# Optimization experiments

Measured on AMD Instinct MI355X. Metric: run time of the kernel, lower is better.

The kernel has to match this reference:

```python
import jax, jax.numpy as jnp
import numpy as np

B, T, D, H, C = 64, 512, 128, 512, 256  # batch, seq_len, input_dim, rnn_dim, clf hidden


def _lstm_cell(x, h, c, Wih, Whh, b):
    # PyTorch gate order: i, f, g, o; b = bias_ih + bias_hh
    gates = x @ Wih.T + h @ Whh.T + b  # [B, 4H]
    i, f, g, o = jnp.split(gates, 4, axis=-1)
    c = jax.nn.sigmoid(f) * c + jax.nn.sigmoid(i) * jnp.tanh(g)
    h = jax.nn.sigmoid(o) * jnp.tanh(c)
    return h, c


def _run_lstm2(xs, state, p0, p1):
    # xs: [B, T, in]; state: (h0, c0, h1, c1) each [B, H]
    def step(carry, x_t):
        h0, c0, h1, c1 = carry
        h0, c0 = _lstm_cell(x_t, h0, c0, *p0)
        h1, c1 = _lstm_cell(h0, h1, c1, *p1)
        return (h0, c0, h1, c1), h1
    state, ys = jax.lax.scan(step, state, jnp.swapaxes(xs, 0, 1))
    return jnp.swapaxes(ys, 0, 1), state


def setup_inputs() -> dict:
    key = jax.random.key(0)
    ks = jax.random.split(key, 18)
    s = 0.04  # ~1/sqrt(H), matches torch LSTM init scale
    w = lambda k, shape: (jax.random.normal(k, shape, jnp.float32) * s)
    inp = {
        "x": jax.random.uniform(ks[0], (B, T, D), dtype=jnp.float32),
        "y": (jax.random.uniform(ks[1], (B, T, D), dtype=jnp.float32) > 0.9).astype(jnp.float32),
        "enc_Wih0": w(ks[2], (4 * H, D)), "enc_Whh0": w(ks[3], (4 * H, H)), "enc_b0": w(ks[4], (4 * H,)),
        "enc_Wih1": w(ks[5], (4 * H, H)), "enc_Whh1": w(ks[6], (4 * H, H)), "enc_b1": w(ks[7], (4 * H,)),
        "dec_Wih0": w(ks[8], (4 * H, D)), "dec_Whh0": w(ks[9], (4 * H, H)), "dec_b0": w(ks[10], (4 * H,)),
        "dec_Wih1": w(ks[11], (4 * H, H)), "dec_Whh1": w(ks[12], (4 * H, H)), "dec_b1": w(ks[13], (4 * H,)),
        "clf_W1": w(ks[14], (C, H)), "clf_b1": w(ks[15], (C,)),
        "clf_W2": w(ks[16], (D, C)), "clf_b2": w(ks[17], (D,)),
    }
    return inp


def reference(x, y, enc_Wih0, enc_Whh0, enc_b0, enc_Wih1, enc_Whh1, enc_b1,
              dec_Wih0, dec_Whh0, dec_b0, dec_Wih1, dec_Whh1, dec_b1,
              clf_W1, clf_b1, clf_W2, clf_b2):
    Bc = x.shape[0]
    z = jnp.zeros((Bc, H), x.dtype)
    # encoder: only final (h, c) of both layers is used
    _, state = _run_lstm2(x, (z, z, z, z),
                          (enc_Wih0, enc_Whh0, enc_b0), (enc_Wih1, enc_Whh1, enc_b1))
    # decoder under full teacher forcing: steps t=1..T-1 consume y[:, t-1]
    dec_out, _ = _run_lstm2(y[:, :-1], state,
                            (dec_Wih0, dec_Whh0, dec_b0), (dec_Wih1, dec_Whh1, dec_b1))
    hid = jax.nn.relu(dec_out @ clf_W1.T + clf_b1)          # [B, T-1, C]
    logits = hid @ clf_W2.T + clf_b2                        # [B, T-1, D]
    # outputs[:, 0] stays zero, as in the torch loop starting at t=1
    return jnp.concatenate([jnp.zeros_like(logits[:, :1]), logits], axis=1)
```

## Files before the change

### kernel.cpp

```cpp
#include <hip/hip_runtime.h>
#include <hip/hip_bf16.h>
#include <stdint.h>

#define SMEM_BYTES 148480

using short8 = __attribute__((ext_vector_type(8))) short;
using f32x4  = __attribute__((ext_vector_type(4))) float;

#define OXBF 0u
#define OYBF 8388608u
#define OWE0 16777216u
#define OWD0 (OWE0 + 2621440u)
#define OWE1 (OWD0 + 2621440u)
#define OWD1 (OWE1 + 4194304u)
#define OWC1 (OWD1 + 4194304u)
#define OWC2 (OWC1 + 262144u)
#define OH0  (OWC2 + 65536u)
#define OH1  (OH0 + 524288u)
#define OHP  (OH1 + 524288u)
#define OFLG (OHP + 262144u)
#define OFC0 (OFLG)
#define OFC1 (OFLG + 4096u)
#define OFH  (OFLG + 8192u)
#define OFL  (OFLG + 9216u)

static __device__ __forceinline__ unsigned short f2bf(float f){
  union { float f; unsigned u; } v; v.f = f;
  unsigned r = v.u + 0x7FFFu + ((v.u >> 16) & 1u);
  return (unsigned short)(r >> 16);
}
static __device__ __forceinline__ float sigm(float x){ return 1.f/(1.f+__expf(-x)); }
static __device__ __forceinline__ float tanh_(float x){ return 1.f - 2.f/(__expf(2.f*x)+1.f); }

static __device__ __forceinline__ uint4 ld_cg16(const void* p){
  uint4 v;
  asm volatile("global_load_dwordx4 %0, %1, off sc0 sc1" : "=v"(v) : "v"(p) : "memory");
  return v;
}
static __device__ __forceinline__ unsigned ld_cg4(const void* p){
  unsigned v;
  asm volatile("global_load_dword %0, %1, off sc0 sc1\n\ts_waitcnt vmcnt(0)"
               : "=v"(v) : "v"(p) : "memory");
  return v;
}
static __device__ __forceinline__ void st_cg2(void* p, unsigned short s){
  unsigned v = s;
  asm volatile("global_store_short %0, %1, off sc0 sc1" :: "v"(p), "v"(v) : "memory");
}
static __device__ __forceinline__ void st_cg4(void* p, unsigned v){
  asm volatile("global_store_dword %0, %1, off sc0 sc1" :: "v"(p), "v"(v) : "memory");
}
static __device__ __forceinline__ void drain_vm(){
  asm volatile("s_waitcnt vmcnt(0)" ::: "memory");
}

__global__ void k_init(float* __restrict__ out, uint8_t* __restrict__ ws){
  int i = blockIdx.x*blockDim.x + threadIdx.x;
  int ns = gridDim.x*blockDim.x;
  uint32_t* z = (uint32_t*)(ws + OH0);
  const int n32 = (int)((OFLG + 16384u - OH0)/4u);
  for (int k=i; k<n32; k+=ns) z[k] = 0u;
  for (int k=i; k<64*128; k+=ns) out[(size_t)(k>>7)*(512*128) + (k&127)] = 0.f;
}

__global__ void k_cvt(const float* __restrict__ x, const float* __restrict__ y,
                      uint8_t* __restrict__ ws){
  unsigned short* xb = (unsigned short*)(ws + OXBF);
  unsigned short* yb = (unsigned short*)(ws + OYBF);
  const int n = 64*512*128;
  int i = blockIdx.x*blockDim.x + threadIdx.x, ns = gridDim.x*blockDim.x;
  for (int k=i; k<n; k+=ns){ xb[k] = f2bf(x[k]); yb[k] = f2bf(y[k]); }
}

__global__ void k_swzgate(const float* __restrict__ Wih, const float* __restrict__ Whh,
                          uint8_t* __restrict__ ws, size_t dstOff, int Kin, int KC, int NKK, int mode){
  unsigned short* dst = (unsigned short*)(ws + dstOff);
  const int total = 2048 * (KC*4);
  int i = blockIdx.x*blockDim.x + threadIdx.x, ns = gridDim.x*blockDim.x;
  for (int idx=i; idx<total; idx+=ns){
    int j = idx & 7;
    int lane = (idx >> 3) & 63;
    int t = idx >> 9;
    int g = t & 3; t >>= 2;
    int kk = t % NKK; t /= NKK;
    int w = t & 3; int ub = t >> 2;
    int off = ((lane>>4)<<3) + j;
    int k = mode ? (kk==0 ? w*32 + off : 128 + w*128 + (kk-1)*32 + off)
                 : (w*KC + kk*32 + off);
    int u = ub*16 + (lane&15);
    int row = g*512 + u;
    float v = (k < Kin) ? Wih[(size_t)row*Kin + k] : Whh[(size_t)row*512 + (k-Kin)];
    dst[idx] = f2bf(v);
  }
}

__global__ void k_swzclf(const float* __restrict__ W, uint8_t* __restrict__ ws,
                         size_t dstOff, int nwgs, int Kw, int Ktot){
  unsigned short* dst = (unsigned short*)(ws + dstOff);
  const int NKK = Kw/32;
  const int total = nwgs*4*NKK*64*8;
  int i = blockIdx.x*blockDim.x + threadIdx.x, ns = gridDim.x*blockDim.x;
  for (int idx=i; idx<total; idx+=ns){
    int j = idx & 7;
    int lane = (idx >> 3) & 63;
    int t = idx >> 9;
    int kk = t % NKK; t /= NKK;
    int w = t & 3; int wg = t >> 2;
    int k = w*Kw + kk*32 + ((lane>>4)<<3) + j;
    int col = wg*16 + (lane&15);
    dst[idx] = f2bf(W[(size_t)col*Ktot + k]);
  }
}

__launch_bounds__(256, 1)
__global__ void k_seq(uint8_t* __restrict__ ws,
                      const float* __restrict__ eb0, const float* __restrict__ eb1,
                      const float* __restrict__ db0, const float* __restrict__ db1,
                      const float* __restrict__ cb1, const float* __restrict__ cb2,
                      float* __restrict__ out){
  __shared__ uint8_t smem[SMEM_BYTES];
  const int wg = blockIdx.x, tid = threadIdx.x;
  const int w = tid>>6, l = tid&63, lr = l&15, lg = l>>4;

  const unsigned short* xb = (const unsigned short*)(ws+OXBF);
  const unsigned short* yb = (const unsigned short*)(ws+OYBF);
  unsigned short* h0r = (unsigned short*)(ws+OH0);
  unsigned short* h1r = (unsigned short*)(ws+OH1);
  unsigned short* hpr = (unsigned short*)(ws+OHP);

  short8* BL = (short8*)smem;
  float*  P0 = (float*)(smem + 131072);
  float*  P1 = (float*)(smem + 139776);

  auto loadB = [&](size_t srcOff, int bytes){
    const uint4* s = (const uint4*)(ws + srcOff);
    uint4* d = (uint4*)smem;
    for (int i = tid; i < bytes/16; i += 256) d[i] = s[i];
  };
  auto pollge = [&](uint32_t baseOff, int n, int tgt, int tb){
    if (tgt > 0 && tid >= tb && tid < tb+n){
      const void* p = (const void*)(ws + baseOff + (size_t)(tid-tb)*64);
      while ((int)ld_cg4(p) < tgt) __builtin_amdgcn_s_sleep(2);
    }
  };
  auto setflag = [&](uint32_t slotOff, int val){
    drain_vm();
    __syncthreads();
    if (tid == 0) st_cg4(ws + slotOff, (unsigned)val);
  };

  if (wg < 128){
    const bool isC0 = wg < 64;
    const int cwg = isC0 ? wg : wg-64;
    const int bt = cwg>>5, ub = cwg&31;
    const int u = tid&15, ug = ub*16 + u;
    const int bbytes = isC0 ? 81920 : 131072;
    const uint32_t myflag = (isC0 ? OFC0 : OFC1) + (uint32_t)(bt*32+ub)*64u;

    float be[4], bd[4];
    {
      const float* e = isC0 ? eb0 : eb1;
      const float* d = isC0 ? db0 : db1;
      #pragma unroll
      for (int g=0; g<4; ++g){ be[g] = e[g*512+ug]; bd[g] = d[g*512+ug]; }
    }
    loadB((isC0 ? (size_t)OWE0 : (size_t)OWE1) + (size_t)ub*bbytes, bbytes);
    float cS0 = 0.f, cS1 = 0.f;
    __syncthreads();

    for (int t = 0; t < 1023; ++t){
      if (t == 512){
        __syncthreads();
        loadB((isC0 ? (size_t)OWD0 : (size_t)OWD1) + (size_t)ub*bbytes, bbytes);
      }
      if (isC0){
        pollge(OFC0 + bt*2048u, 32, t, 0);
        pollge(OFC1 + bt*2048u, 32, t-7, 32);
      } else {
        pollge(OFC0 + bt*2048u, 32, t+1, 0);
        pollge(OFC1 + bt*2048u, 32, t, 32);
        pollge(OFH, 16, t-519, 64);
      }
      __syncthreads();

      const int slotW = t&7, slotR = (t+7)&7;
      f32x4 acc[2][4];
      #pragma unroll
      for (int m=0;m<2;++m)
        #pragma unroll
        for (int g=0;g<4;++g) acc[m][g] = (f32x4){0.f,0.f,0.f,0.f};

      if (isC0){
        const unsigned short* xs = (t<512) ? xb : yb;
        const int tt = (t<512) ? t : t-512;
        short8 ax[2];
        uint4 ah[4][2];
        #pragma unroll
        for (int m=0;m<2;++m){
          const int b = bt*32 + m*16 + lr;
          ax[m] = *(const short8*)(xs + ((size_t)b*512 + tt)*128 + w*32 + (lg<<3));
          #pragma unroll
          for (int kk=1; kk<5; ++kk)
            ah[kk-1][m] = ld_cg16(h0r + ((size_t)slotR*64 + b)*512 + w*128 + (kk-1)*32 + (lg<<3));
        }
        drain_vm();
        __builtin_amdgcn_sched_barrier(0);
        #pragma unroll
        for (int g=0;g<4;++g){
          short8 bf = BL[((w*5+0)*4+g)*64 + l];
          acc[0][g] = __builtin_amdgcn_mfma_f32_16x16x32_bf16(ax[0], bf, acc[0][g],0,0,0);
          acc[1][g] = __builtin_amdgcn_mfma_f32_16x16x32_bf16(ax[1], bf, acc[1][g],0,0,0);
        }
        #pragma unroll
        for (int kk=1; kk<5; ++kk)
          #pragma unroll
          for (int g=0;g<4;++g){
            short8 bf = BL[((w*5+kk)*4+g)*64 + l];
            acc[0][g] = __builtin_amdgcn_mfma_f32_16x16x32_bf16(__builtin_bit_cast(short8, ah[kk-1][0]), bf, acc[0][g],0,0,0);
            acc[1][g] = __builtin_amdgcn_mfma_f32_16x16x32_bf16(__builtin_bit_cast(short8, ah[kk-1][1]), bf, acc[1][g],0,0,0);
          }
      } else {
        uint4 a[8][2];
        #pragma unroll
        for (int kk=0; kk<8; ++kk){
          const int k0 = w*256 + kk*32;
          #pragma unroll
          for (int m=0;m<2;++m){
            const int b = bt*32 + m*16 + lr;
            const void* ap = (k0 < 512)
              ? (const void*)(h0r + ((size_t)slotW*64 + b)*512 + k0 + (lg<<3))
              : (const void*)(h1r + ((size_t)slotR*64 + b)*512 + (k0-512) + (lg<<3));
            a[kk][m] = ld_cg16(ap);
          }
        }
        drain_vm();
        __builtin_amdgcn_sched_barrier(0);
        #pragma unroll
        for (int kk=0; kk<8; ++kk)
          #pragma unroll
          for (int g=0;g<4;++g){
            short8 bf = BL[((w*8+kk)*4+g)*64 + l];
            acc[0][g] = __builtin_amdgcn_mfma_f32_16x16x32_bf16(__builtin_bit_cast(short8, a[kk][0]), bf, acc[0][g],0,0,0);
            acc[1][g] = __builtin_amdgcn_mfma_f32_16x16x32_bf16(__builtin_bit_cast(short8, a[kk][1]), bf, acc[1][g],0,0,0);
          }
      }

      {
        float* P = (w&1) ? P1 : P0;
        if (w < 2){
          #pragma unroll
          for (int m=0;m<2;++m)
            #pragma unroll
            for (int g=0;g<4;++g)
              #pragma unroll
              for (int r=0;r<4;++r)
                P[(m*16 + (lg<<2) + r)*68 + g*16 + lr] = acc[m][g][r];
        }
        __syncthreads();
        if (w >= 2){
          #pragma unroll
          for (int m=0;m<2;++m)
            #pragma unroll
            for (int g=0;g<4;++g)
              #pragma unroll
              for (int r=0;r<4;++r)
                P[(m*16 + (lg<<2) + r)*68 + g*16 + lr] += acc[m][g][r];
        }
        __syncthreads();
      }

      const float* bias = (t<512) ? be : bd;
      unsigned short* hout = isC0 ? h0r : h1r;
      #pragma unroll
      for (int s=0;s<2;++s){
        const int row = (tid>>4) + s*16;
        const int pi = row*68 + u;
        float gi = P0[pi]      + P1[pi]      + bias[0];
        float gf = P0[pi+16]   + P1[pi+16]   + bias[1];
        float gg = P0[pi+32]   + P1[pi+32]   + bias[2];
        float go = P0[pi+48]   + P1[pi+48]   + bias[3];
        float cprev = s ? cS1 : cS0;
        float c = sigm(gf)*cprev + sigm(gi)*tanh_(gg);
        if (s) cS1 = c; else cS0 = c;
        float h = sigm(go)*tanh_(c);
        st_cg2(hout + ((size_t)slotW*64 + (bt*32+row))*512 + ug, f2bf(h));
      }
      setflag(myflag, t+1);
    }
  } else if (wg < 144){
    const int hwg = wg - 128;
    const int u = tid&15, col = hwg*16 + u;
    const float bc = cb1[col];
    loadB((size_t)OWC1 + (size_t)hwg*16384, 16384);
    __syncthreads();
    for (int t2 = 0; t2 < 511; ++t2){
      pollge(OFC1, 64, 513+t2, 0);
      pollge(OFL, 8, t2-7, 64);
      __syncthreads();
      const int slot = (512+t2)&7, slw = t2&7;
      f32x4 ha[4];
      #pragma unroll
      for (int m=0;m<4;++m) ha[m] = (f32x4){0.f,0.f,0.f,0.f};
      uint4 a[4][4];
      #pragma unroll
      for (int kk=0; kk<4; ++kk)
        #pragma unroll
        for (int m=0;m<4;++m)
          a[kk][m] = ld_cg16(h1r + ((size_t)slot*64 + m*16+lr)*512 + w*128 + kk*32 + (lg<<3));
      drain_vm();
      __builtin_amdgcn_sched_barrier(0);
      #pragma unroll
      for (int kk=0; kk<4; ++kk){
        short8 bf = BL[(w*4+kk)*64 + l];
        #pragma unroll
        for (int m=0;m<4;++m)
          ha[m] = __builtin_amdgcn_mfma_f32_16x16x32_bf16(__builtin_bit_cast(short8, a[kk][m]), bf, ha[m],0,0,0);
      }
      {
        float* P = (w&1) ? P1 : P0;
        if (w < 2){
          #pragma unroll
          for (int m=0;m<4;++m)
            #pragma unroll
            for (int r=0;r<4;++r)
              P[(m*16 + (lg<<2) + r)*20 + lr] = ha[m][r];
        }
        __syncthreads();
        if (w >= 2){
          #pragma unroll
          for (int m=0;m<4;++m)
            #pragma unroll
            for (int r=0;r<4;++r)
              P[(m*16 + (lg<<2) + r)*20 + lr] += ha[m][r];
        }
        __syncthreads();
      }
      #pragma unroll
      for (int s=0;s<4;++s){
        const int row = (tid>>4) + s*16;
        float v = P0[row*20+u] + P1[row*20+u] + bc;
        v = fmaxf(v, 0.f);
        st_cg2(hpr + ((size_t)slw*64 + row)*256 + col, f2bf(v));
      }
      setflag(OFH + (uint32_t)hwg*64u, t2+1);
    }
  } else if (wg < 152){
    const int lwg = wg - 144;
    const int u = tid&15, col = lwg*16 + u;
    const float bc = cb2[col];
    loadB((size_t)OWC2 + (size_t)lwg*8192, 8192);
    __syncthreads();
    for (int t3 = 0; t3 < 511; ++t3){
      pollge(OFH, 16, t3+1, 0);
      __syncthreads();
      const int slot = t3&7;
      f32x4 la[4];
      #pragma unroll
      for (int m=0;m<4;++m) la[m] = (f32x4){0.f,0.f,0.f,0.f};
      uint4 a[2][4];
      #pragma unroll
      for (int kk=0; kk<2; ++kk)
        #pragma unroll
        for (int m=0;m<4;++m)
          a[kk][m] = ld_cg16(hpr + ((size_t)slot*64 + m*16+lr)*256 + w*64 + kk*32 + (lg<<3));
      drain_vm();
      __builtin_amdgcn_sched_barrier(0);
      #pragma unroll
      for (int kk=0; kk<2; ++kk){
        short8 bf = BL[(w*2+kk)*64 + l];
        #pragma unroll
        for (int m=0;m<4;++m)
          la[m] = __builtin_amdgcn_mfma_f32_16x16x32_bf16(__builtin_bit_cast(short8, a[kk][m]), bf, la[m],0,0,0);
      }
      {
        float* P = (w&1) ? P1 : P0;
        if (w < 2){
          #pragma unroll
          for (int m=0;m<4;++m)
            #pragma unroll
            for (int r=0;r<4;++r)
              P[(m*16 + (lg<<2) + r)*20 + lr] = la[m][r];
        }
        __syncthreads();
        if (w >= 2){
          #pragma unroll
          for (int m=0;m<4;++m)
            #pragma unroll
            for (int r=0;r<4;++r)
              P[(m*16 + (lg<<2) + r)*20 + lr] += la[m][r];
        }
        __syncthreads();
      }
      #pragma unroll
      for (int s=0;s<4;++s){
        const int row = (tid>>4) + s*16;
        float v = P0[row*20+u] + P1[row*20+u] + bc;
        out[((size_t)row*512 + (t3+1))*128 + col] = v;
      }
      setflag(OFL + (uint32_t)lwg*64u, t3+1);
    }
  }
}

extern "C" void kernel_launch(void* const* d_in, const int* in_sizes, int n_in,
                              void* d_out, int out_size, void* d_ws, size_t ws_size,
                              hipStream_t stream){
  const float* x   = (const float*)d_in[0];
  const float* y   = (const float*)d_in[1];
  const float* eW0 = (const float*)d_in[2];
  const float* eU0 = (const float*)d_in[3];
  const float* eb0 = (const float*)d_in[4];
  const float* eW1 = (const float*)d_in[5];
  const float* eU1 = (const float*)d_in[6];
  const float* eb1 = (const float*)d_in[7];
  const float* dW0 = (const float*)d_in[8];
  const float* dU0 = (const float*)d_in[9];
  const float* db0 = (const float*)d_in[10];
  const float* dW1 = (const float*)d_in[11];
  const float* dU1 = (const float*)d_in[12];
  const float* db1 = (const float*)d_in[13];
  const float* cW1 = (const float*)d_in[14];
  const float* cb1 = (const float*)d_in[15];
  const float* cW2 = (const float*)d_in[16];
  const float* cb2 = (const float*)d_in[17];
  float* out = (float*)d_out;
  uint8_t* ws = (uint8_t*)d_ws;
  (void)in_sizes; (void)n_in; (void)out_size; (void)ws_size;

  k_init<<<dim3(256), dim3(256), 0, stream>>>(out, ws);
  k_cvt<<<dim3(2048), dim3(256), 0, stream>>>(x, y, ws);
  k_swzgate<<<dim3(1280), dim3(256), 0, stream>>>(eW0, eU0, ws, (size_t)OWE0, 128, 160, 5, 1);
  k_swzgate<<<dim3(1280), dim3(256), 0, stream>>>(dW0, dU0, ws, (size_t)OWD0, 128, 160, 5, 1);
  k_swzgate<<<dim3(2048), dim3(256), 0, stream>>>(eW1, eU1, ws, (size_t)OWE1, 512, 256, 8, 0);
  k_swzgate<<<dim3(2048), dim3(256), 0, stream>>>(dW1, dU1, ws, (size_t)OWD1, 512, 256, 8, 0);
  k_swzclf<<<dim3(256), dim3(256), 0, stream>>>(cW1, ws, (size_t)OWC1, 16, 128, 512);
  k_swzclf<<<dim3(64),  dim3(256), 0, stream>>>(cW2, ws, (size_t)OWC2, 8, 64, 256);
  k_seq<<<dim3(152), dim3(256), 0, stream>>>(ws, eb0, eb1, db0, db1, cb1, cb2, out);
}
```

Before: 5.310 ms.

## Replace flag polling with sentinel-tagged data slots for inter-workgroup handoff

Ring-buffer slots for hidden states are pre-filled with an all-ones sentinel, and consumers spin on the data loads themselves until no sentinel remains. This removes most per-step flag writes, the drain-plus-barrier before each flag, and the separate flag polls on the critical recurrent path. Producers stage h in LDS and publish it with 16-byte stores, and each consumer clears a slot two steps ahead. Flags stay only for back-pressure, and a separate h1 buffer is added for the decoder phase. The risks are torn 16-byte reads, a real bf16 value equal to 0xFFFF (a NaN pattern), and races between clearing and reading slots.

After: 5.639 ms. 1.06x slower.

```diff
diff --git a/kernel.cpp b/kernel.cpp
--- a/kernel.cpp
+++ b/kernel.cpp
@@ -2,10 +2,11 @@
 #include <hip/hip_bf16.h>
 #include <stdint.h>
 
-#define SMEM_BYTES 148480
-
-using short8 = __attribute__((ext_vector_type(8))) short;
-using f32x4  = __attribute__((ext_vector_type(4))) float;
+#define SMEM_BYTES 150528
+
+using short8  = __attribute__((ext_vector_type(8))) short;
+using f32x4   = __attribute__((ext_vector_type(4))) float;
+using u32x4   = __attribute__((ext_vector_type(4))) unsigned int;
 
 #define OXBF 0u
 #define OYBF 8388608u
@@ -19,10 +20,10 @@
 #define OH1  (OH0 + 524288u)
 #define OHP  (OH1 + 524288u)
 #define OFLG (OHP + 262144u)
-#define OFC0 (OFLG)
 #define OFC1 (OFLG + 4096u)
 #define OFH  (OFLG + 8192u)
 #define OFL  (OFLG + 9216u)
+#define OH1B (OFLG + 16384u)
 
 static __device__ __forceinline__ unsigned short f2bf(float f){
   union { float f; unsigned u; } v; v.f = f;
@@ -32,8 +33,8 @@
 static __device__ __forceinline__ float sigm(float x){ return 1.f/(1.f+__expf(-x)); }
 static __device__ __forceinline__ float tanh_(float x){ return 1.f - 2.f/(__expf(2.f*x)+1.f); }
 
-static __device__ __forceinline__ uint4 ld_cg16(const void* p){
-  uint4 v;
+static __device__ __forceinline__ u32x4 ld_cg16(const void* p){
+  u32x4 v;
   asm volatile("global_load_dwordx4 %0, %1, off sc0 sc1" : "=v"(v) : "v"(p) : "memory");
   return v;
 }
@@ -43,23 +44,35 @@
                : "=v"(v) : "v"(p) : "memory");
   return v;
 }
-static __device__ __forceinline__ void st_cg2(void* p, unsigned short s){
-  unsigned v = s;
-  asm volatile("global_store_short %0, %1, off sc0 sc1" :: "v"(p), "v"(v) : "memory");
+static __device__ __forceinline__ void st_cg16(void* p, u32x4 v){
+  asm volatile("global_store_dwordx4 %0, %1, off sc0 sc1" :: "v"(p), "v"(v) : "memory");
 }
 static __device__ __forceinline__ void st_cg4(void* p, unsigned v){
   asm volatile("global_store_dword %0, %1, off sc0 sc1" :: "v"(p), "v"(v) : "memory");
 }
 static __device__ __forceinline__ void drain_vm(){
   asm volatile("s_waitcnt vmcnt(0)" ::: "memory");
+}
+static __device__ __forceinline__ bool isS(u32x4 v){
+  return (v[0]==0xFFFFFFFFu) | (v[1]==0xFFFFFFFFu) | (v[2]==0xFFFFFFFFu) | (v[3]==0xFFFFFFFFu);
 }
 
 __global__ void k_init(float* __restrict__ out, uint8_t* __restrict__ ws){
   int i = blockIdx.x*blockDim.x + threadIdx.x;
   int ns = gridDim.x*blockDim.x;
-  uint32_t* z = (uint32_t*)(ws + OH0);
-  const int n32 = (int)((OFLG + 16384u - OH0)/4u);
-  for (int k=i; k<n32; k+=ns) z[k] = 0u;
+  uint32_t* r0 = (uint32_t*)(ws + OH0);
+  uint32_t* r1 = (uint32_t*)(ws + OH1);
+  const int slotw = 65536/4;
+  for (int k=i; k<8*slotw; k+=ns){
+    unsigned v = (k < 7*slotw) ? 0xFFFFFFFFu : 0u;
+    r0[k] = v; r1[k] = v;
+  }
+  uint32_t* rb = (uint32_t*)(ws + OH1B);
+  for (int k=i; k<8*slotw; k+=ns) rb[k] = 0xFFFFFFFFu;
+  uint32_t* rp = (uint32_t*)(ws + OHP);
+  for (int k=i; k<262144/4; k+=ns) rp[k] = 0xFFFFFFFFu;
+  uint32_t* fl = (uint32_t*)(ws + OFLG);
+  for (int k=i; k<16384/4; k+=ns) fl[k] = 0u;
   for (int k=i; k<64*128; k+=ns) out[(size_t)(k>>7)*(512*128) + (k&127)] = 0.f;
 }
 
@@ -126,27 +139,20 @@
   const unsigned short* yb = (const unsigned short*)(ws+OYBF);
   unsigned short* h0r = (unsigned short*)(ws+OH0);
   unsigned short* h1r = (unsigned short*)(ws+OH1);
+  unsigned short* h1b = (unsigned short*)(ws+OH1B);
   unsigned short* hpr = (unsigned short*)(ws+OHP);
 
   short8* BL = (short8*)smem;
   float*  P0 = (float*)(smem + 131072);
   float*  P1 = (float*)(smem + 139776);
+  unsigned short* HS = (unsigned short*)(smem + 148480);
+
+  const u32x4 S4 = (u32x4){0xFFFFFFFFu,0xFFFFFFFFu,0xFFFFFFFFu,0xFFFFFFFFu};
 
   auto loadB = [&](size_t srcOff, int bytes){
-    const uint4* s = (const uint4*)(ws + srcOff);
-    uint4* d = (uint4*)smem;
+    const u32x4* s = (const u32x4*)(ws + srcOff);
+    u32x4* d = (u32x4*)smem;
     for (int i = tid; i < bytes/16; i += 256) d[i] = s[i];
-  };
-  auto pollge = [&](uint32_t baseOff, int n, int tgt, int tb){
-    if (tgt > 0 && tid >= tb && tid < tb+n){
-      const void* p = (const void*)(ws + baseOff + (size_t)(tid-tb)*64);
-      while ((int)ld_cg4(p) < tgt) __builtin_amdgcn_s_sleep(2);
-    }
-  };
-  auto setflag = [&](uint32_t slotOff, int val){
-    drain_vm();
-    __syncthreads();
-    if (tid == 0) st_cg4(ws + slotOff, (unsigned)val);
   };
 
   if (wg < 128){
@@ -155,7 +161,6 @@
     const int bt = cwg>>5, ub = cwg&31;
     const int u = tid&15, ug = ub*16 + u;
     const int bbytes = isC0 ? 81920 : 131072;
-    const uint32_t myflag = (isC0 ? OFC0 : OFC1) + (uint32_t)(bt*32+ub)*64u;
 
     float be[4], bd[4];
     {
@@ -172,16 +177,27 @@
       if (t == 512){
         __syncthreads();
         loadB((isC0 ? (size_t)OWD0 : (size_t)OWD1) + (size_t)ub*bbytes, bbytes);
-      }
-      if (isC0){
-        pollge(OFC0 + bt*2048u, 32, t, 0);
-        pollge(OFC1 + bt*2048u, 32, t-7, 32);
-      } else {
-        pollge(OFC0 + bt*2048u, 32, t+1, 0);
-        pollge(OFC1 + bt*2048u, 32, t, 32);
-        pollge(OFH, 16, t-519, 64);
-      }
-      __syncthreads();
+        __syncthreads();
+      }
+
+      unsigned short* pub_base = isC0 ? h0r : ((t >= 512) ? h1b : h1r);
+      unsigned short* clr_base = isC0 ? h0r : ((t+2 >= 512) ? h1b : h1r);
+
+      if (w == 0){
+        if (isC0){
+          if (t >= 6 && l < 32){
+            const void* p = ws + OFC1 + (size_t)(bt*32+l)*64;
+            while ((int)ld_cg4(p) < t-5) __builtin_amdgcn_s_sleep(2);
+          }
+        } else {
+          if (t >= 518 && l < 16){
+            const void* p = ws + OFH + (size_t)l*64;
+            while ((int)ld_cg4(p) < t-517) __builtin_amdgcn_s_sleep(2);
+          }
+        }
+        const int cs = (t+2)&7, row = l>>1, half = l&1;
+        st_cg16(clr_base + ((size_t)cs*64 + bt*32 + row)*512 + ub*16 + half*8, S4);
+      }
 
       const int slotW = t&7, slotR = (t+7)&7;
       f32x4 acc[2][4];
@@ -194,16 +210,31 @@
         const unsigned short* xs = (t<512) ? xb : yb;
         const int tt = (t<512) ? t : t-512;
         short8 ax[2];
-        uint4 ah[4][2];
         #pragma unroll
         for (int m=0;m<2;++m){
           const int b = bt*32 + m*16 + lr;
           ax[m] = *(const short8*)(xs + ((size_t)b*512 + tt)*128 + w*32 + (lg<<3));
-          #pragma unroll
-          for (int kk=1; kk<5; ++kk)
-            ah[kk-1][m] = ld_cg16(h0r + ((size_t)slotR*64 + b)*512 + w*128 + (kk-1)*32 + (lg<<3));
-        }
-        drain_vm();
+        }
+        u32x4 ah[4][2];
+        const unsigned short* base = h0r + (size_t)slotR*64*512;
+        bool bad;
+        do {
+          #pragma unroll
+          for (int kk=0; kk<4; ++kk)
+            #pragma unroll
+            for (int m=0;m<2;++m){
+              const int b = bt*32 + m*16 + lr;
+              ah[kk][m] = ld_cg16(base + (size_t)b*512 + w*128 + kk*32 + (lg<<3));
+            }
+          drain_vm();
+          __builtin_amdgcn_sched_barrier(0);
+          bad = false;
+          #pragma unroll
+          for (int kk=0; kk<4; ++kk)
+            #pragma unroll
+            for (int m=0;m<2;++m) bad |= isS(ah[kk][m]);
+          if (bad) __builtin_amdgcn_s_sleep(1);
+        } while (bad);
         __builtin_amdgcn_sched_barrier(0);
         #pragma unroll
         for (int g=0;g<4;++g){
@@ -220,20 +251,32 @@
             acc[1][g] = __builtin_amdgcn_mfma_f32_16x16x32_bf16(__builtin_bit_cast(short8, ah[kk-1][1]), bf, acc[1][g],0,0,0);
           }
       } else {
-        uint4 a[8][2];
-        #pragma unroll
-        for (int kk=0; kk<8; ++kk){
-          const int k0 = w*256 + kk*32;
-          #pragma unroll
-          for (int m=0;m<2;++m){
-            const int b = bt*32 + m*16 + lr;
-            const void* ap = (k0 < 512)
-              ? (const void*)(h0r + ((size_t)slotW*64 + b)*512 + k0 + (lg<<3))
-              : (const void*)(h1r + ((size_t)slotR*64 + b)*512 + (k0-512) + (lg<<3));
-            a[kk][m] = ld_cg16(ap);
+        u32x4 a[8][2];
+        const unsigned short* b0 = h0r + (size_t)slotW*64*512;
+        const unsigned short* b1 = ((t-1 >= 512) ? h1b : h1r) + (size_t)slotR*64*512;
+        bool bad;
+        do {
+          #pragma unroll
+          for (int kk=0; kk<8; ++kk){
+            const int k0 = w*256 + kk*32;
+            #pragma unroll
+            for (int m=0;m<2;++m){
+              const int b = bt*32 + m*16 + lr;
+              const void* ap = (k0 < 512)
+                ? (const void*)(b0 + (size_t)b*512 + k0 + (lg<<3))
+                : (const void*)(b1 + (size_t)b*512 + (k0-512) + (lg<<3));
+              a[kk][m] = ld_cg16(ap);
+            }
           }
-        }
-        drain_vm();
+          drain_vm();
+          __builtin_amdgcn_sched_barrier(0);
+          bad = false;
+          #pragma unroll
+          for (int kk=0; kk<8; ++kk)
+            #pragma unroll
+            for (int m=0;m<2;++m) bad |= isS(a[kk][m]);
+          if (bad) __builtin_amdgcn_s_sleep(1);
+        } while (bad);
         __builtin_amdgcn_sched_barrier(0);
         #pragma unroll
         for (int kk=0; kk<8; ++kk)
@@ -270,7 +313,6 @@
       }
 
       const float* bias = (t<512) ? be : bd;
-      unsigned short* hout = isC0 ? h0r : h1r;
       #pragma unroll
       for (int s=0;s<2;++s){
         const int row = (tid>>4) + s*16;
@@ -283,9 +325,16 @@
         float c = sigm(gf)*cprev + sigm(gi)*tanh_(gg);
         if (s) cS1 = c; else cS0 = c;
         float h = sigm(go)*tanh_(c);
-        st_cg2(hout + ((size_t)slotW*64 + (bt*32+row))*512 + ug, f2bf(h));
-      }
-      setflag(myflag, t+1);
+        HS[row*16 + u] = f2bf(h);
+      }
+      __syncthreads();
+      if (tid < 64){
+        u32x4 v = *(const u32x4*)(HS + tid*8);
+        const int row = tid>>1, half = tid&1;
+        st_cg16(pub_base + ((size_t)slotW*64 + bt*32 + row)*512 + ub*16 + half*8, v);
+      }
+      if (!isC0 && tid == 0)
+        st_cg4(ws + OFC1 + (size_t)(bt*32+ub)*64, (unsigned)(t+1));
     }
   } else if (wg < 144){
     const int hwg = wg - 128;
@@ -294,21 +343,41 @@
     loadB((size_t)OWC1 + (size_t)hwg*16384, 16384);
     __syncthreads();
     for (int t2 = 0; t2 < 511; ++t2){
-      pollge(OFC1, 64, 513+t2, 0);
-      pollge(OFL, 8, t2-7, 64);
-      __syncthreads();
-      const int slot = (512+t2)&7, slw = t2&7;
+      if (w == 0){
+        if (t2 >= 6 && l < 8){
+          const void* p = ws + OFL + (size_t)l*64;
+          while ((int)ld_cg4(p) < t2-5) __builtin_amdgcn_s_sleep(2);
+        }
+        const int cs = (t2+2)&7;
+        #pragma unroll
+        for (int q=0;q<2;++q){
+          const int i = l*2+q, row = i>>1, half = i&1;
+          st_cg16(hpr + ((size_t)cs*64 + row)*256 + hwg*16 + half*8, S4);
+        }
+      }
+      const int slot = t2&7;
+      u32x4 a[4][4];
+      const unsigned short* base = h1b + (size_t)slot*64*512;
+      bool bad;
+      do {
+        #pragma unroll
+        for (int kk=0; kk<4; ++kk)
+          #pragma unroll
+          for (int m=0;m<4;++m)
+            a[kk][m] = ld_cg16(base + (size_t)(m*16+lr)*512 + w*128 + kk*32 + (lg<<3));
+        drain_vm();
+        __builtin_amdgcn_sched_barrier(0);
+        bad = false;
+        #pragma unroll
+        for (int kk=0; kk<4; ++kk)
+          #pragma unroll
+          for (int m=0;m<4;++m) bad |= isS(a[kk][m]);
+        if (bad) __builtin_amdgcn_s_sleep(1);
+      } while (bad);
+      __builtin_amdgcn_sched_barrier(0);
       f32x4 ha[4];
       #pragma unroll
       for (int m=0;m<4;++m) ha[m] = (f32x4){0.f,0.f,0.f,0.f};
-      uint4 a[4][4];
-      #pragma unroll
-      for (int kk=0; kk<4; ++kk)
-        #pragma unroll
-        for (int m=0;m<4;++m)
-          a[kk][m] = ld_cg16(h1r + ((size_t)slot*64 + m*16+lr)*512 + w*128 + kk*32 + (lg<<3));
-      drain_vm();
-      __builtin_amdgcn_sched_barrier(0);
       #pragma unroll
       for (int kk=0; kk<4; ++kk){
         short8 bf = BL[(w*4+kk)*64 + l];
@@ -339,10 +408,15 @@
       for (int s=0;s<4;++s){
         const int row = (tid>>4) + s*16;
         float v = P0[row*20+u] + P1[row*20+u] + bc;
-        v = fmaxf(v, 0.f);
-        st_cg2(hpr + ((size_t)slw*64 + row)*256 + col, f2bf(v));
-      }
-      setflag(OFH + (uint32_t)hwg*64u, t2+1);
+        HS[row*16 + u] = f2bf(fmaxf(v, 0.f));
+      }
+      __syncthreads();
+      if (tid < 128){
+        u32x4 v = *(const u32x4*)(HS + tid*8);
+        const int row = tid>>1, half = tid&1;
+        st_cg16(hpr + ((size_t)slot*64 + row)*256 + hwg*16 + half*8, v);
+      }
+      if (tid == 0) st_cg4(ws + OFH + (size_t)hwg*64, (unsigned)(t2+1));
     }
   } else if (wg < 152){
     const int lwg = wg - 144;
@@ -351,20 +425,29 @@
     loadB((size_t)OWC2 + (size_t)lwg*8192, 8192);
     __syncthreads();
     for (int t3 = 0; t3 < 511; ++t3){
-      pollge(OFH, 16, t3+1, 0);
-      __syncthreads();
       const int slot = t3&7;
+      u32x4 a[2][4];
+      const unsigned short* base = hpr + (size_t)slot*64*256;
+      bool bad;
+      do {
+        #pragma unroll
+        for (int kk=0; kk<2; ++kk)
+          #pragma unroll
+          for (int m=0;m<4;++m)
+            a[kk][m] = ld_cg16(base + (size_t)(m*16+lr)*256 + w*64 + kk*32 + (lg<<3));
+        drain_vm();
+        __builtin_amdgcn_sched_barrier(0);
+        bad = false;
+        #pragma unroll
+        for (int kk=0; kk<2; ++kk)
+          #pragma unroll
+          for (int m=0;m<4;++m) bad |= isS(a[kk][m]);
+        if (bad) __builtin_amdgcn_s_sleep(1);
+      } while (bad);
+      __builtin_amdgcn_sched_barrier(0);
       f32x4 la[4];
       #pragma unroll
       for (int m=0;m<4;++m) la[m] = (f32x4){0.f,0.f,0.f,0.f};
-      uint4 a[2][4];
-      #pragma unroll
-      for (int kk=0; kk<2; ++kk)
-        #pragma unroll
-        for (int m=0;m<4;++m)
-          a[kk][m] = ld_cg16(hpr + ((size_t)slot*64 + m*16+lr)*256 + w*64 + kk*32 + (lg<<3));
-      drain_vm();
-      __builtin_amdgcn_sched_barrier(0);
       #pragma unroll
       for (int kk=0; kk<2; ++kk){
         short8 bf = BL[(w*2+kk)*64 + l];
@@ -397,7 +480,7 @@
         float v = P0[row*20+u] + P1[row*20+u] + bc;
         out[((size_t)row*512 + (t3+1))*128 + col] = v;
       }
-      setflag(OFL + (uint32_t)lwg*64u, t3+1);
+      if (tid == 0) st_cg4(ws + OFL + (size_t)lwg*64, (unsigned)(t3+1));
     }
   }
 }
```
